# Optimization experiments

Hardware: AMD Instinct MI355X
Metric: run time of the kernel (lower is better)

The kernel has to match this reference:

```python
import jax, jax.numpy as jnp
import numpy as np

DIM = 256
HEADS = 4
DIM_HEADS = 32
HIDDEN = HEADS * DIM_HEADS


def setup_inputs() -> dict:
    key = jax.random.key(0)
    k0, k1, k2, k3, k4, k5, k6 = jax.random.split(key, 7)
    b, c, h, w = 16, DIM, 64, 64
    s = 1.0 / np.sqrt(DIM)
    return {
        "x": jax.random.normal(k0, (b, c, h, w), dtype=jnp.float32),
        "Wq": jax.random.normal(k1, (HIDDEN, DIM), dtype=jnp.float32) * s,
        "Wk": jax.random.normal(k2, (HIDDEN, DIM), dtype=jnp.float32) * s,
        "Wv": jax.random.normal(k3, (HIDDEN, DIM), dtype=jnp.float32) * s,
        "Wo": jax.random.normal(k4, (DIM, HIDDEN), dtype=jnp.float32) / np.sqrt(HIDDEN),
        "bo": jax.random.normal(k5, (DIM,), dtype=jnp.float32) * 0.01,
        "g": jnp.ones((DIM,), dtype=jnp.float32),
    }


def reference(x, Wq, Wk, Wv, Wo, bo, g):
    b, c, h, w = x.shape
    n = h * w
    scale = DIM_HEADS ** (-0.5)
    xf = x.reshape(b, c, n)  # [b,c,n]
    # 1x1 convs == channel matmuls
    q = jnp.einsum('dc,bcn->bdn', Wq, xf).reshape(b, HEADS, DIM_HEADS, n)
    k = jnp.einsum('dc,bcn->bdn', Wk, xf).reshape(b, HEADS, DIM_HEADS, n)
    v = jnp.einsum('dc,bcn->bdn', Wv, xf).reshape(b, HEADS, DIM_HEADS, n)
    q = jax.nn.softmax(q, axis=-2) * scale  # softmax over head-dim
    k = jax.nn.softmax(k, axis=-1)          # softmax over tokens
    v = v / n
    context = jnp.einsum('bhdn,bhen->bhde', k, v)  # [b,h,dh,dh]
    out = jnp.einsum('bhde,bhdn->bhen', context, q)  # [b,h,dh,n]
    out = out.reshape(b, HIDDEN, n)
    out = jnp.einsum('cd,bdn->bcn', Wo, out) + bo[None, :, None]
    # LayerNorm over channel dim (biased var, eps=1e-5 for fp32)
    eps = 1e-5
    mean = jnp.mean(out, axis=1, keepdims=True)
    var = jnp.var(out, axis=1, keepdims=True)
    out = (out - mean) * jax.lax.rsqrt(var + eps) * g[None, :, None]
    return out.reshape(b, c, h, w)
```

## Files before the change

kernel.cpp:

```cpp
#include <hip/hip_runtime.h>
#include <hip/hip_bf16.h>

typedef float f32x4 __attribute__((ext_vector_type(4)));
typedef short bf16x8 __attribute__((ext_vector_type(8)));
typedef unsigned short us4 __attribute__((ext_vector_type(4)));

#define NB 16
#define NC 256
#define NTOK 4096
#define NHID 128

__device__ __forceinline__ unsigned pk2(float lo, float hi) {
  float2 f; f.x = lo; f.y = hi;
  __hip_bfloat162 h = __float22bfloat162_rn(f);
  unsigned u; __builtin_memcpy(&u, &h, 4); return u;
}
__device__ __forceinline__ unsigned short f2bf(float f) {
  __hip_bfloat16 h = __float2bfloat16(f);
  unsigned short u; __builtin_memcpy(&u, &h, 2); return u;
}
__device__ __forceinline__ uint2 pk4(f32x4 v) {
  uint2 r; r.x = pk2(v[0], v[1]); r.y = pk2(v[2], v[3]); return r;
}
__device__ __forceinline__ float bf2f(unsigned short h) {
  union { unsigned u; float f; } v; v.u = ((unsigned)h) << 16;
  return v.f;
}

__global__ __launch_bounds__(512) void k0_w(
    const float* __restrict__ Wq, const float* __restrict__ Wk,
    const float* __restrict__ Wv, unsigned short* __restrict__ Wswz)
{
  const int mt = blockIdx.x;
  const int t = threadIdx.x;
  const int ks = t >> 6, l = t & 63;
  const int m = mt * 16 + (l & 15);
  const int col = ks * 32 + (l >> 4) * 8;
  const float* src = (m < 128) ? (Wq + (size_t)m * NC)
                   : (m < 256) ? (Wk + (size_t)(m - 128) * NC)
                               : (Wv + (size_t)(m - 256) * NC);
  const float4 w0 = *(const float4*)(src + col);
  const float4 w1 = *(const float4*)(src + col + 4);
  uint4 p;
  p.x = pk2(w0.x, w0.y); p.y = pk2(w0.z, w0.w);
  p.z = pk2(w1.x, w1.y); p.w = pk2(w1.z, w1.w);
  *(uint4*)&Wswz[((size_t)(mt * 8 + ks)) * 512 + l * 8] = p;
}

__global__ __launch_bounds__(512, 4) void k1_qkv(
    const float* __restrict__ x, const unsigned short* __restrict__ Wswz,
    unsigned short* __restrict__ qswz, unsigned short* __restrict__ Pp,
    float* __restrict__ Sp)
{
  __shared__ __align__(16) unsigned char smem[49152];

  const int tile = blockIdx.x, b = blockIdx.y;
  const int n0 = tile * 64;
  const int t = threadIdx.x;
  const int wid = t >> 6, l = t & 63;
  const int l16 = l & 15, lhi = l >> 4;
  const unsigned xr = (unsigned)((l16 & 7) << 4);

  int fr[3];
  if (wid < 4) { fr[0] = 2 * wid; fr[1] = 2 * wid + 1; fr[2] = 8 + wid; }
  else { const int w = wid - 4; fr[0] = 12 + w; fr[1] = 16 + 2 * w; fr[2] = 17 + 2 * w; }

  {
    const int slot = t & 15;
    const int cp0 = t >> 4;
    const float* xb = x + ((size_t)b * NC) * NTOK + n0;
#pragma unroll
    for (int i = 0; i < 4; ++i) {
      const int c0 = 2 * (cp0 + 32 * i);
      const float4 a0 = *(const float4*)(xb + (size_t)c0 * NTOK + slot * 4);
      const float4 a1 = *(const float4*)(xb + (size_t)(c0 + 1) * NTOK + slot * 4);
      const float* p0 = (const float*)&a0;
      const float* p1 = (const float*)&a1;
#pragma unroll
      for (int j = 0; j < 4; ++j) {
        const int tok = slot * 4 + j;
        const unsigned off = (unsigned)(tok * 512 + 2 * c0) ^ ((unsigned)(tok & 7) << 4);
        *(unsigned*)(smem + off) = pk2(p0[j], p1[j]);
      }
    }
  }
  __syncthreads();

#define WFRAG(f, kss) (*(const bf16x8*)&Wswz[((size_t)(fr[f] * 8 + (kss))) * 512 + l * 8])
#define AFRAG(tf, kss) (*(const bf16x8*)(smem + \
    (((unsigned)(((tf) * 16 + l16) * 512 + (kss) * 64 + lhi * 16)) ^ xr)))

  f32x4 acc[4][3];
#pragma unroll
  for (int i = 0; i < 4; ++i)
#pragma unroll
    for (int j = 0; j < 3; ++j) acc[i][j] = 0;

  bf16x8 w0[3], w1[3];
#pragma unroll
  for (int f = 0; f < 3; ++f) w0[f] = WFRAG(f, 0);

#pragma unroll
  for (int kk = 0; kk < 4; ++kk) {
    const int ke = 2 * kk, ko = 2 * kk + 1;
#pragma unroll
    for (int f = 0; f < 3; ++f) w1[f] = WFRAG(f, ko);
#pragma unroll
    for (int tf = 0; tf < 4; ++tf) {
      const bf16x8 a = AFRAG(tf, ke);
#pragma unroll
      for (int f = 0; f < 3; ++f)
        acc[tf][f] = __builtin_amdgcn_mfma_f32_16x16x32_bf16(a, w0[f], acc[tf][f], 0, 0, 0);
    }
    if (kk < 3) {
#pragma unroll
      for (int f = 0; f < 3; ++f) w0[f] = WFRAG(f, ke + 2);
    }
#pragma unroll
    for (int tf = 0; tf < 4; ++tf) {
      const bf16x8 a = AFRAG(tf, ko);
#pragma unroll
      for (int f = 0; f < 3; ++f)
        acc[tf][f] = __builtin_amdgcn_mfma_f32_16x16x32_bf16(a, w1[f], acc[tf][f], 0, 0, 0);
    }
  }

  const float qscale = 0.1767766952966369f;
  if (wid < 4) {
#pragma unroll
    for (int tf = 0; tf < 4; ++tf)
#pragma unroll
      for (int r = 0; r < 4; ++r) {
        const float a0 = acc[tf][0][r], a1 = acc[tf][1][r];
        float mx = fmaxf(a0, a1);
        mx = fmaxf(mx, __shfl_xor(mx, 1));
        mx = fmaxf(mx, __shfl_xor(mx, 2));
        mx = fmaxf(mx, __shfl_xor(mx, 4));
        mx = fmaxf(mx, __shfl_xor(mx, 8));
        const float e0 = __expf(a0 - mx), e1 = __expf(a1 - mx);
        float s = e0 + e1;
        s += __shfl_xor(s, 1); s += __shfl_xor(s, 2);
        s += __shfl_xor(s, 4); s += __shfl_xor(s, 8);
        const float inv = qscale / s;
        acc[tf][0][r] = e0 * inv;
        acc[tf][1][r] = e1 * inv;
      }
    float s = 0.f;
#pragma unroll
    for (int tf = 0; tf < 4; ++tf)
#pragma unroll
      for (int r = 0; r < 4; ++r) {
        const float e = __expf(acc[tf][2][r]);
        acc[tf][2][r] = e;
        s += e;
      }
    s += __shfl_xor(s, 16);
    s += __shfl_xor(s, 32);
    if (l < 16) Sp[((size_t)b * 64 + tile) * 128 + (fr[2] - 8) * 16 + l16] = s;
  } else {
    float s = 0.f;
#pragma unroll
    for (int tf = 0; tf < 4; ++tf)
#pragma unroll
      for (int r = 0; r < 4; ++r) {
        const float e = __expf(acc[tf][0][r]);
        acc[tf][0][r] = e;
        s += e;
      }
    s += __shfl_xor(s, 16);
    s += __shfl_xor(s, 32);
    if (l < 16) Sp[((size_t)b * 64 + tile) * 128 + (fr[0] - 8) * 16 + l16] = s;
  }
  __syncthreads();

  if (wid < 4) {
#pragma unroll
    for (int f = 0; f < 2; ++f) {
      const int j = fr[f] * 16 + l16;
#pragma unroll
      for (int tf = 0; tf < 4; ++tf)
#pragma unroll
        for (int r = 0; r < 4; ++r) {
          const int tok = tf * 16 + lhi * 4 + r;
          const unsigned off = 32768u + (unsigned)(tok * 256) +
                               (((unsigned)(2 * j)) ^ ((unsigned)(tok & 7) << 4));
          *(unsigned short*)(smem + off) = f2bf(acc[tf][f][r]);
        }
    }
    const int row = (fr[2] - 8) * 16 + l16;
#pragma unroll
    for (int tf = 0; tf < 4; ++tf)
      *(uint2*)(smem + (((unsigned)(row * 128 + tf * 32 + lhi * 8)) ^ xr)) = pk4(acc[tf][2]);
  } else {
    const int rowk = (fr[0] - 8) * 16 + l16;
    const int rowv1 = 128 + (fr[1] - 16) * 16 + l16;
    const int rowv2 = 128 + (fr[2] - 16) * 16 + l16;
#pragma unroll
    for (int tf = 0; tf < 4; ++tf) {
      *(uint2*)(smem + (((unsigned)(rowk * 128 + tf * 32 + lhi * 8)) ^ xr)) = pk4(acc[tf][0]);
      *(uint2*)(smem + (((unsigned)(rowv1 * 128 + tf * 32 + lhi * 8)) ^ xr)) = pk4(acc[tf][1]);
      *(uint2*)(smem + (((unsigned)(rowv2 * 128 + tf * 32 + lhi * 8)) ^ xr)) = pk4(acc[tf][2]);
    }
  }
  __syncthreads();

  if (wid >= 4) {
    const int h = wid - 4;
    f32x4 ca[2][2];
    ca[0][0] = 0; ca[0][1] = 0; ca[1][0] = 0; ca[1][1] = 0;
#pragma unroll
    for (int ks2 = 0; ks2 < 2; ++ks2) {
      bf16x8 ae[2], be[2];
#pragma unroll
      for (int d = 0; d < 2; ++d)
        ae[d] = *(const bf16x8*)(smem +
            (((unsigned)((h * 32 + d * 16 + l16) * 128 + ks2 * 64 + lhi * 16)) ^ xr));
#pragma unroll
      for (int e = 0; e < 2; ++e)
        be[e] = *(const bf16x8*)(smem +
            (((unsigned)((128 + h * 32 + e * 16 + l16) * 128 + ks2 * 64 + lhi * 16)) ^ xr));
#pragma unroll
      for (int d = 0; d < 2; ++d)
#pragma unroll
        for (int e = 0; e < 2; ++e)
          ca[d][e] = __builtin_amdgcn_mfma_f32_16x16x32_bf16(ae[d], be[e], ca[d][e], 0, 0, 0);
    }
    unsigned short* pb = Pp + (((size_t)b * 64 + tile) * 4 + h) * 1024;
#pragma unroll
    for (int d = 0; d < 2; ++d)
#pragma unroll
      for (int e = 0; e < 2; ++e)
        *(uint2*)&pb[(e * 16 + l16) * 32 + d * 16 + lhi * 4] = pk4(ca[d][e]);
  } else {
    const int g = wid;
    const int tok = g * 16 + l16;
#pragma unroll
    for (int ks = 0; ks < 4; ++ks) {
      const bf16x8 v = *(const bf16x8*)(smem + 32768u + (unsigned)(tok * 256) +
                          (((unsigned)(ks * 64 + lhi * 16)) ^ xr));
      *(bf16x8*)&qswz[(((size_t)(b * 256 + tile * 4 + g)) * 4 + ks) * 512 + l * 8] = v;
    }
  }
}

__global__ __launch_bounds__(256) void k2a_tree(
    const unsigned short* __restrict__ Pp, const float* __restrict__ Sp,
    float* __restrict__ Pr, float* __restrict__ Sr)
{
  const int seg = blockIdx.x, b = blockIdx.y;
  const int t = threadIdx.x;
  const unsigned short* pb = Pp + ((size_t)b * 64 + seg * 8) * 4096;
  f32x4 a[4];
#pragma unroll
  for (int i = 0; i < 4; ++i) a[i] = 0;
#pragma unroll
  for (int tile = 0; tile < 8; ++tile) {
#pragma unroll
    for (int i = 0; i < 4; ++i) {
      const us4 v = *(const us4*)&pb[tile * 4096 + i * 1024 + t * 4];
      a[i][0] += bf2f(v[0]); a[i][1] += bf2f(v[1]);
      a[i][2] += bf2f(v[2]); a[i][3] += bf2f(v[3]);
    }
  }
  float* pr = Pr + ((size_t)b * 8 + seg) * 4096;
#pragma unroll
  for (int i = 0; i < 4; ++i) *(f32x4*)&pr[i * 1024 + t * 4] = a[i];

  if (t < 128) {
    float s = 0.f;
    const float* sb = Sp + ((size_t)b * 64 + seg * 8) * 128 + t;
#pragma unroll
    for (int i = 0; i < 8; ++i) s += sb[i * 128];
    Sr[((size_t)b * 8 + seg) * 128 + t] = s;
  }
}

__global__ __launch_bounds__(256) void k2b_norm(
    const float* __restrict__ Pr, const float* __restrict__ Sr,
    float* __restrict__ Cn)
{
  __shared__ float Ss[32];
  const int h = blockIdx.x, b = blockIdx.y;
  const int t = threadIdx.x;
  if (t < 32) {
    float s = 0.f;
    const float* sb = Sr + (size_t)b * 8 * 128 + h * 32 + t;
#pragma unroll
    for (int i = 0; i < 8; ++i) s += sb[i * 128];
    Ss[t] = 1.0f / (s * 4096.0f);
  }
  __syncthreads();
  const int e = t >> 3, d4 = (t & 7) * 4;
  f32x4 a = 0;
#pragma unroll
  for (int seg = 0; seg < 8; ++seg) {
    const f32x4 v = *(const f32x4*)&Pr[((size_t)b * 8 + seg) * 4096 + h * 1024 + e * 32 + d4];
#pragma unroll
    for (int j = 0; j < 4; ++j) a[j] += v[j];
  }
  f32x4 o;
#pragma unroll
  for (int j = 0; j < 4; ++j) o[j] = a[j] * Ss[d4 + j];
  *(f32x4*)&Cn[(size_t)b * 4096 + h * 1024 + e * 32 + d4] = o;
}

__global__ __launch_bounds__(256) void k2c_m(
    const float* __restrict__ Wo, const float* __restrict__ Cn,
    unsigned short* __restrict__ Mswz)
{
  const int ct = blockIdx.x, b = blockIdx.y;
  const int t = threadIdx.x;
  const int ks = t >> 6, l = t & 63;
  const int c = ct * 16 + (l & 15);
  const int d0 = (l >> 4) * 8;
  const float* wr = Wo + (size_t)c * NHID + ks * 32;
  const float* cb = Cn + (size_t)b * 4096 + ks * 1024;
  f32x4 s0 = 0, s1 = 0;
#pragma unroll 8
  for (int e = 0; e < 32; ++e) {
    const float w = wr[e];
    const f32x4 c0 = *(const f32x4*)&cb[e * 32 + d0];
    const f32x4 c1 = *(const f32x4*)&cb[e * 32 + d0 + 4];
#pragma unroll
    for (int j = 0; j < 4; ++j) { s0[j] += w * c0[j]; s1[j] += w * c1[j]; }
  }
  uint4 p;
  p.x = pk2(s0[0], s0[1]); p.y = pk2(s0[2], s0[3]);
  p.z = pk2(s1[0], s1[1]); p.w = pk2(s1[2], s1[3]);
  *(uint4*)&Mswz[(((size_t)b * 16 + ct) * 4 + ks) * 512 + l * 8] = p;
}

__global__ __launch_bounds__(256, 3) void k3_out(
    const unsigned short* __restrict__ qswz, const unsigned short* __restrict__ Mswz,
    const float* __restrict__ bo, const float* __restrict__ g, float* __restrict__ out)
{
  __shared__ float red[4 * 64 * 2];
  const int bx = blockIdx.x, b = blockIdx.y;
  const int t = threadIdx.x;
  const int wid = t >> 6, l = t & 63;
  const int l16 = l & 15, lhi = l >> 4;

  bf16x8 mf[4][4];
#pragma unroll
  for (int cf = 0; cf < 4; ++cf)
#pragma unroll
    for (int ks = 0; ks < 4; ++ks)
      mf[cf][ks] = *(const bf16x8*)&Mswz[(((size_t)b * 16 + wid * 4 + cf) * 4 + ks) * 512 + l * 8];

  f32x4 acc[4][4];
#pragma unroll
  for (int i = 0; i < 4; ++i)
#pragma unroll
    for (int j = 0; j < 4; ++j) acc[i][j] = 0;

#pragma unroll
  for (int tf = 0; tf < 4; ++tf) {
    bf16x8 qf[4];
#pragma unroll
    for (int ks = 0; ks < 4; ++ks)
      qf[ks] = *(const bf16x8*)&qswz[(((size_t)(b * 256 + bx * 4 + tf)) * 4 + ks) * 512 + l * 8];
#pragma unroll
    for (int ks = 0; ks < 4; ++ks)
#pragma unroll
      for (int cf = 0; cf < 4; ++cf)
        acc[tf][cf] = __builtin_amdgcn_mfma_f32_16x16x32_bf16(qf[ks], mf[cf][ks], acc[tf][cf], 0, 0, 0);
  }

  float bol[4], gl[4];
#pragma unroll
  for (int cf = 0; cf < 4; ++cf) {
    const int c = wid * 64 + cf * 16 + l16;
    bol[cf] = bo[c]; gl[cf] = g[c];
  }
#pragma unroll
  for (int tf = 0; tf < 4; ++tf)
#pragma unroll
    for (int cf = 0; cf < 4; ++cf)
#pragma unroll
      for (int r = 0; r < 4; ++r) acc[tf][cf][r] += bol[cf];

#pragma unroll
  for (int tf = 0; tf < 4; ++tf)
#pragma unroll
    for (int r = 0; r < 4; ++r) {
      float s = 0.f, q2 = 0.f;
#pragma unroll
      for (int cf = 0; cf < 4; ++cf) {
        const float v = acc[tf][cf][r];
        s += v; q2 += v * v;
      }
      s += __shfl_xor(s, 1); q2 += __shfl_xor(q2, 1);
      s += __shfl_xor(s, 2); q2 += __shfl_xor(q2, 2);
      s += __shfl_xor(s, 4); q2 += __shfl_xor(q2, 4);
      s += __shfl_xor(s, 8); q2 += __shfl_xor(q2, 8);
      if (l16 == 0) {
        const int tok = tf * 16 + lhi * 4 + r;
        red[(wid * 64 + tok) * 2] = s;
        red[(wid * 64 + tok) * 2 + 1] = q2;
      }
    }
  __syncthreads();

  float mean[4][4], rstd[4][4];
#pragma unroll
  for (int tf = 0; tf < 4; ++tf)
#pragma unroll
    for (int r = 0; r < 4; ++r) {
      const int tok = tf * 16 + lhi * 4 + r;
      float s = 0.f, q2 = 0.f;
#pragma unroll
      for (int cg = 0; cg < 4; ++cg) {
        s += red[(cg * 64 + tok) * 2];
        q2 += red[(cg * 64 + tok) * 2 + 1];
      }
      const float mu = s * (1.0f / 256.0f);
      const float var = q2 * (1.0f / 256.0f) - mu * mu;
      mean[tf][r] = mu;
      rstd[tf][r] = rsqrtf(var + 1e-5f);
    }

  float* ob = out + ((size_t)b * NC) * NTOK + bx * 64;
#pragma unroll
  for (int tf = 0; tf < 4; ++tf)
#pragma unroll
    for (int cf = 0; cf < 4; ++cf) {
      const int c = wid * 64 + cf * 16 + l16;
      f32x4 ov;
#pragma unroll
      for (int r = 0; r < 4; ++r)
        ov[r] = (acc[tf][cf][r] - mean[tf][r]) * rstd[tf][r] * gl[cf];
      *(f32x4*)&ob[(size_t)c * NTOK + tf * 16 + lhi * 4] = ov;
    }
}

extern "C" void kernel_launch(void* const* d_in, const int* in_sizes, int n_in,
                              void* d_out, int out_size, void* d_ws, size_t ws_size,
                              hipStream_t stream) {
  const float* x  = (const float*)d_in[0];
  const float* Wq = (const float*)d_in[1];
  const float* Wk = (const float*)d_in[2];
  const float* Wv = (const float*)d_in[3];
  const float* Wo = (const float*)d_in[4];
  const float* bo = (const float*)d_in[5];
  const float* g  = (const float*)d_in[6];
  float* out = (float*)d_out;

  char* ws = (char*)d_ws;
  unsigned short* Wswz = (unsigned short*)(ws);
  unsigned short* qswz = (unsigned short*)(ws + 262144);
  unsigned short* Pp   = (unsigned short*)(ws + 17039360);
  float*          Sp   = (float*)(ws + 25427968);
  float*          Pr   = (float*)(ws + 25952256);
  float*          Sr   = (float*)(ws + 28049408);
  float*          Cn   = (float*)(ws + 28114944);
  unsigned short* Mswz = (unsigned short*)(ws + 28377088);
  (void)ws_size; (void)in_sizes; (void)n_in; (void)out_size;

  hipLaunchKernelGGL(k0_w, dim3(24), dim3(512), 0, stream, Wq, Wk, Wv, Wswz);
  hipLaunchKernelGGL(k1_qkv, dim3(64, NB), dim3(512), 0, stream, x, Wswz, qswz, Pp, Sp);
  hipLaunchKernelGGL(k2a_tree, dim3(8, NB), dim3(256), 0, stream, Pp, Sp, Pr, Sr);
  hipLaunchKernelGGL(k2b_norm, dim3(4, NB), dim3(256), 0, stream, Pr, Sr, Cn);
  hipLaunchKernelGGL(k2c_m, dim3(16, NB), dim3(256), 0, stream, Wo, Cn, Mswz);
  hipLaunchKernelGGL(k3_out, dim3(64, NB), dim3(256), 0, stream, qswz, Mswz, bo, g, out);
}
```

Measured before the change: 78.28 us.

## Restructure q handoff, fuse context normalize into M build, rebalance context MFMA

k1 now writes q directly from registers to global in a plain per-tile layout instead of staging it through an extra 16 KB of shared memory, which shrinks LDS use and cuts shared traffic. The x load is rewritten to read 8 channel rows per thread and pack 16-byte LDS stores. The k·v context MFMA is spread across all 8 waves instead of 4. The normalize and M-build kernels are merged into one launch that keeps the normalized context in shared memory, while k3 now stages q through LDS with scalar 2-byte gathers, which adds shared-memory work and two barriers in the output kernel.

After: 77.36 us. No clear change (-1.2%).

```diff
diff --git a/kernel.cpp b/kernel.cpp
--- a/kernel.cpp
+++ b/kernel.cpp
@@ -14,10 +14,6 @@
   float2 f; f.x = lo; f.y = hi;
   __hip_bfloat162 h = __float22bfloat162_rn(f);
   unsigned u; __builtin_memcpy(&u, &h, 4); return u;
-}
-__device__ __forceinline__ unsigned short f2bf(float f) {
-  __hip_bfloat16 h = __float2bfloat16(f);
-  unsigned short u; __builtin_memcpy(&u, &h, 2); return u;
 }
 __device__ __forceinline__ uint2 pk4(f32x4 v) {
   uint2 r; r.x = pk2(v[0], v[1]); r.y = pk2(v[2], v[3]); return r;
@@ -49,10 +45,10 @@
 
 __global__ __launch_bounds__(512, 4) void k1_qkv(
     const float* __restrict__ x, const unsigned short* __restrict__ Wswz,
-    unsigned short* __restrict__ qswz, unsigned short* __restrict__ Pp,
+    unsigned short* __restrict__ qg, unsigned short* __restrict__ Pp,
     float* __restrict__ Sp)
 {
-  __shared__ __align__(16) unsigned char smem[49152];
+  __shared__ __align__(16) unsigned char smem[32768];
 
   const int tile = blockIdx.x, b = blockIdx.y;
   const int n0 = tile * 64;
@@ -66,22 +62,19 @@
   else { const int w = wid - 4; fr[0] = 12 + w; fr[1] = 16 + 2 * w; fr[2] = 17 + 2 * w; }
 
   {
-    const int slot = t & 15;
-    const int cp0 = t >> 4;
-    const float* xb = x + ((size_t)b * NC) * NTOK + n0;
-#pragma unroll
-    for (int i = 0; i < 4; ++i) {
-      const int c0 = 2 * (cp0 + 32 * i);
-      const float4 a0 = *(const float4*)(xb + (size_t)c0 * NTOK + slot * 4);
-      const float4 a1 = *(const float4*)(xb + (size_t)(c0 + 1) * NTOK + slot * 4);
-      const float* p0 = (const float*)&a0;
-      const float* p1 = (const float*)&a1;
-#pragma unroll
-      for (int j = 0; j < 4; ++j) {
-        const int tok = slot * 4 + j;
-        const unsigned off = (unsigned)(tok * 512 + 2 * c0) ^ ((unsigned)(tok & 7) << 4);
-        *(unsigned*)(smem + off) = pk2(p0[j], p1[j]);
-      }
+    const int cg = t >> 4;
+    const int tq = t & 15;
+    const float* rp = x + (size_t)b * NC * NTOK + (size_t)(cg * 8) * NTOK + n0 + tq * 4;
+    float4 rv[8];
+#pragma unroll
+    for (int i = 0; i < 8; ++i) rv[i] = *(const float4*)(rp + (size_t)i * NTOK);
+#pragma unroll
+    for (int j = 0; j < 4; ++j) {
+      const int tok = tq * 4 + j;
+      uint4 pv;
+      pv.x = pk2(rv[0][j], rv[1][j]); pv.y = pk2(rv[2][j], rv[3][j]);
+      pv.z = pk2(rv[4][j], rv[5][j]); pv.w = pk2(rv[6][j], rv[7][j]);
+      *(uint4*)(smem + (((unsigned)(tok * 512 + cg * 16)) ^ ((unsigned)(tok & 7) << 4))) = pv;
     }
   }
   __syncthreads();
@@ -157,6 +150,15 @@
     s += __shfl_xor(s, 16);
     s += __shfl_xor(s, 32);
     if (l < 16) Sp[((size_t)b * 64 + tile) * 128 + (fr[2] - 8) * 16 + l16] = s;
+
+    unsigned short* qt = qg + ((size_t)(b * 64 + tile)) * 8192;
+#pragma unroll
+    for (int f = 0; f < 2; ++f) {
+      const int j = fr[f] * 16 + l16;
+#pragma unroll
+      for (int tf = 0; tf < 4; ++tf)
+        *(uint2*)&qt[tf * 2048 + j * 16 + lhi * 4] = pk4(acc[tf][f]);
+    }
   } else {
     float s = 0.f;
 #pragma unroll
@@ -174,19 +176,6 @@
   __syncthreads();
 
   if (wid < 4) {
-#pragma unroll
-    for (int f = 0; f < 2; ++f) {
-      const int j = fr[f] * 16 + l16;
-#pragma unroll
-      for (int tf = 0; tf < 4; ++tf)
-#pragma unroll
-        for (int r = 0; r < 4; ++r) {
-          const int tok = tf * 16 + lhi * 4 + r;
-          const unsigned off = 32768u + (unsigned)(tok * 256) +
-                               (((unsigned)(2 * j)) ^ ((unsigned)(tok & 7) << 4));
-          *(unsigned short*)(smem + off) = f2bf(acc[tf][f][r]);
-        }
-    }
     const int row = (fr[2] - 8) * 16 + l16;
 #pragma unroll
     for (int tf = 0; tf < 4; ++tf)
@@ -204,42 +193,25 @@
   }
   __syncthreads();
 
-  if (wid >= 4) {
-    const int h = wid - 4;
-    f32x4 ca[2][2];
-    ca[0][0] = 0; ca[0][1] = 0; ca[1][0] = 0; ca[1][1] = 0;
+  {
+    const int h = wid & 3, dh = wid >> 2;
+    f32x4 ca[2];
+    ca[0] = 0; ca[1] = 0;
 #pragma unroll
     for (int ks2 = 0; ks2 < 2; ++ks2) {
-      bf16x8 ae[2], be[2];
-#pragma unroll
-      for (int d = 0; d < 2; ++d)
-        ae[d] = *(const bf16x8*)(smem +
-            (((unsigned)((h * 32 + d * 16 + l16) * 128 + ks2 * 64 + lhi * 16)) ^ xr));
-#pragma unroll
-      for (int e = 0; e < 2; ++e)
-        be[e] = *(const bf16x8*)(smem +
+      const bf16x8 ae = *(const bf16x8*)(smem +
+          (((unsigned)((h * 32 + dh * 16 + l16) * 128 + ks2 * 64 + lhi * 16)) ^ xr));
+#pragma unroll
+      for (int e = 0; e < 2; ++e) {
+        const bf16x8 be = *(const bf16x8*)(smem +
             (((unsigned)((128 + h * 32 + e * 16 + l16) * 128 + ks2 * 64 + lhi * 16)) ^ xr));
-#pragma unroll
-      for (int d = 0; d < 2; ++d)
-#pragma unroll
-        for (int e = 0; e < 2; ++e)
-          ca[d][e] = __builtin_amdgcn_mfma_f32_16x16x32_bf16(ae[d], be[e], ca[d][e], 0, 0, 0);
+        ca[e] = __builtin_amdgcn_mfma_f32_16x16x32_bf16(ae, be, ca[e], 0, 0, 0);
+      }
     }
     unsigned short* pb = Pp + (((size_t)b * 64 + tile) * 4 + h) * 1024;
 #pragma unroll
-    for (int d = 0; d < 2; ++d)
-#pragma unroll
-      for (int e = 0; e < 2; ++e)
-        *(uint2*)&pb[(e * 16 + l16) * 32 + d * 16 + lhi * 4] = pk4(ca[d][e]);
-  } else {
-    const int g = wid;
-    const int tok = g * 16 + l16;
-#pragma unroll
-    for (int ks = 0; ks < 4; ++ks) {
-      const bf16x8 v = *(const bf16x8*)(smem + 32768u + (unsigned)(tok * 256) +
-                          (((unsigned)(ks * 64 + lhi * 16)) ^ xr));
-      *(bf16x8*)&qswz[(((size_t)(b * 256 + tile * 4 + g)) * 4 + ks) * 512 + l * 8] = v;
-    }
+    for (int e = 0; e < 2; ++e)
+      *(uint2*)&pb[(e * 16 + l16) * 32 + dh * 16 + lhi * 4] = pk4(ca[e]);
   }
 }
 
@@ -275,46 +247,39 @@
   }
 }
 
-__global__ __launch_bounds__(256) void k2b_norm(
+__global__ __launch_bounds__(256) void k2bc(
     const float* __restrict__ Pr, const float* __restrict__ Sr,
-    float* __restrict__ Cn)
+    const float* __restrict__ Wo, unsigned short* __restrict__ Mswz)
 {
-  __shared__ float Ss[32];
-  const int h = blockIdx.x, b = blockIdx.y;
+  __shared__ float CnS[4096];
+  __shared__ float Ss[128];
+  const int ct = blockIdx.x, b = blockIdx.y;
   const int t = threadIdx.x;
-  if (t < 32) {
+
+  if (t < 128) {
     float s = 0.f;
-    const float* sb = Sr + (size_t)b * 8 * 128 + h * 32 + t;
+    const float* sb = Sr + (size_t)b * 8 * 128 + t;
 #pragma unroll
     for (int i = 0; i < 8; ++i) s += sb[i * 128];
     Ss[t] = 1.0f / (s * 4096.0f);
   }
   __syncthreads();
-  const int e = t >> 3, d4 = (t & 7) * 4;
-  f32x4 a = 0;
-#pragma unroll
-  for (int seg = 0; seg < 8; ++seg) {
-    const f32x4 v = *(const f32x4*)&Pr[((size_t)b * 8 + seg) * 4096 + h * 1024 + e * 32 + d4];
-#pragma unroll
-    for (int j = 0; j < 4; ++j) a[j] += v[j];
-  }
-  f32x4 o;
-#pragma unroll
-  for (int j = 0; j < 4; ++j) o[j] = a[j] * Ss[d4 + j];
-  *(f32x4*)&Cn[(size_t)b * 4096 + h * 1024 + e * 32 + d4] = o;
-}
-
-__global__ __launch_bounds__(256) void k2c_m(
-    const float* __restrict__ Wo, const float* __restrict__ Cn,
-    unsigned short* __restrict__ Mswz)
-{
-  const int ct = blockIdx.x, b = blockIdx.y;
-  const int t = threadIdx.x;
+
+#pragma unroll
+  for (int i = 0; i < 16; ++i) {
+    const int idx = t + 256 * i;
+    float a = 0.f;
+#pragma unroll
+    for (int seg = 0; seg < 8; ++seg) a += Pr[((size_t)b * 8 + seg) * 4096 + idx];
+    CnS[idx] = a * Ss[((idx >> 10) << 5) | (idx & 31)];
+  }
+  __syncthreads();
+
   const int ks = t >> 6, l = t & 63;
   const int c = ct * 16 + (l & 15);
   const int d0 = (l >> 4) * 8;
   const float* wr = Wo + (size_t)c * NHID + ks * 32;
-  const float* cb = Cn + (size_t)b * 4096 + ks * 1024;
+  const float* cb = &CnS[ks * 1024];
   f32x4 s0 = 0, s1 = 0;
 #pragma unroll 8
   for (int e = 0; e < 32; ++e) {
@@ -331,15 +296,23 @@
 }
 
 __global__ __launch_bounds__(256, 3) void k3_out(
-    const unsigned short* __restrict__ qswz, const unsigned short* __restrict__ Mswz,
+    const unsigned short* __restrict__ qg, const unsigned short* __restrict__ Mswz,
     const float* __restrict__ bo, const float* __restrict__ g, float* __restrict__ out)
 {
+  __shared__ __align__(16) unsigned char qs[16384];
   __shared__ float red[4 * 64 * 2];
   const int bx = blockIdx.x, b = blockIdx.y;
   const int t = threadIdx.x;
   const int wid = t >> 6, l = t & 63;
   const int l16 = l & 15, lhi = l >> 4;
 
+  {
+    const unsigned char* gq = (const unsigned char*)(qg + ((size_t)(b * 64 + bx)) * 8192);
+#pragma unroll
+    for (int i = 0; i < 4; ++i)
+      *(uint4*)(qs + t * 16 + i * 4096) = *(const uint4*)(gq + t * 16 + i * 4096);
+  }
+
   bf16x8 mf[4][4];
 #pragma unroll
   for (int cf = 0; cf < 4; ++cf)
@@ -353,12 +326,22 @@
 #pragma unroll
     for (int j = 0; j < 4; ++j) acc[i][j] = 0;
 
+  __syncthreads();
+
 #pragma unroll
   for (int tf = 0; tf < 4; ++tf) {
     bf16x8 qf[4];
 #pragma unroll
-    for (int ks = 0; ks < 4; ++ks)
-      qf[ks] = *(const bf16x8*)&qswz[(((size_t)(b * 256 + bx * 4 + tf)) * 4 + ks) * 512 + l * 8];
+    for (int ks = 0; ks < 4; ++ks) {
+      bf16x8 qv;
+#pragma unroll
+      for (int jj = 0; jj < 8; ++jj) {
+        const unsigned short u = *(const unsigned short*)(qs +
+            tf * 4096 + (ks * 32 + lhi * 8 + jj) * 32 + l16 * 2);
+        qv[jj] = (short)u;
+      }
+      qf[ks] = qv;
+    }
 #pragma unroll
     for (int ks = 0; ks < 4; ++ks)
 #pragma unroll
@@ -378,6 +361,8 @@
     for (int cf = 0; cf < 4; ++cf)
 #pragma unroll
       for (int r = 0; r < 4; ++r) acc[tf][cf][r] += bol[cf];
+
+  __syncthreads();
 
 #pragma unroll
   for (int tf = 0; tf < 4; ++tf)
@@ -447,19 +432,17 @@
 
   char* ws = (char*)d_ws;
   unsigned short* Wswz = (unsigned short*)(ws);
-  unsigned short* qswz = (unsigned short*)(ws + 262144);
+  unsigned short* qg   = (unsigned short*)(ws + 262144);
   unsigned short* Pp   = (unsigned short*)(ws + 17039360);
   float*          Sp   = (float*)(ws + 25427968);
   float*          Pr   = (float*)(ws + 25952256);
   float*          Sr   = (float*)(ws + 28049408);
-  float*          Cn   = (float*)(ws + 28114944);
   unsigned short* Mswz = (unsigned short*)(ws + 28377088);
   (void)ws_size; (void)in_sizes; (void)n_in; (void)out_size;
 
   hipLaunchKernelGGL(k0_w, dim3(24), dim3(512), 0, stream, Wq, Wk, Wv, Wswz);
-  hipLaunchKernelGGL(k1_qkv, dim3(64, NB), dim3(512), 0, stream, x, Wswz, qswz, Pp, Sp);
+  hipLaunchKernelGGL(k1_qkv, dim3(64, NB), dim3(512), 0, stream, x, Wswz, qg, Pp, Sp);
   hipLaunchKernelGGL(k2a_tree, dim3(8, NB), dim3(256), 0, stream, Pp, Sp, Pr, Sr);
-  hipLaunchKernelGGL(k2b_norm, dim3(4, NB), dim3(256), 0, stream, Pr, Sr, Cn);
-  hipLaunchKernelGGL(k2c_m, dim3(16, NB), dim3(256), 0, stream, Wo, Cn, Mswz);
-  hipLaunchKernelGGL(k3_out, dim3(64, NB), dim3(256), 0, stream, qswz, Mswz, bo, g, out);
-}
+  hipLaunchKernelGGL(k2bc, dim3(16, NB), dim3(256), 0, stream, Pr, Sr, Wo, Mswz);
+  hipLaunchKernelGGL(k3_out, dim3(64, NB), dim3(256), 0, stream, qg, Mswz, bo, g, out);
+}
```
